# Kernel tuning notes

Hardware: AMD Instinct MI355X
Metric: run time of the kernel (lower is better)

The kernel has to match this reference:

```python
import jax, jax.numpy as jnp
import numpy as np

COST_CLASS, COST_BBOX, COST_GIOU = 1.0, 5.0, 2.0

def box_cxcywh_to_xyxy(b):
    cx, cy, w, h = b[..., 0], b[..., 1], b[..., 2], b[..., 3]
    return jnp.stack([cx - 0.5 * w, cy - 0.5 * h, cx + 0.5 * w, cy + 0.5 * h], axis=-1)

def generalized_box_iou(b1, b2):
    # b1: [bs, Q, 4] xyxy, b2: [bs, T, 4] xyxy -> [bs, Q, T]
    area1 = (b1[..., 2] - b1[..., 0]) * (b1[..., 3] - b1[..., 1])  # [bs,Q]
    area2 = (b2[..., 2] - b2[..., 0]) * (b2[..., 3] - b2[..., 1])  # [bs,T]
    b1e = b1[:, :, None, :]  # [bs,Q,1,4]
    b2e = b2[:, None, :, :]  # [bs,1,T,4]
    lt = jnp.maximum(b1e[..., :2], b2e[..., :2])
    rb = jnp.minimum(b1e[..., 2:], b2e[..., 2:])
    wh = jnp.clip(rb - lt, 0.0)
    inter = wh[..., 0] * wh[..., 1]                       # [bs,Q,T]
    union = area1[:, :, None] + area2[:, None, :] - inter
    iou = inter / union
    # smallest enclosing box
    lt_e = jnp.minimum(b1e[..., :2], b2e[..., :2])
    rb_e = jnp.maximum(b1e[..., 2:], b2e[..., 2:])
    wh_e = jnp.clip(rb_e - lt_e, 0.0)
    area_e = wh_e[..., 0] * wh_e[..., 1]
    return iou - (area_e - union) / area_e

def setup_inputs() -> dict:
    key = jax.random.key(0)
    k1, k2, k3, k4 = jax.random.split(key, 4)
    bs, Q, T, C = 256, 300, 100, 92
    return {
        "pred_logits": jax.random.normal(k1, (bs, Q, C), dtype=jnp.float32),
        "pred_boxes": jax.random.uniform(k2, (bs, Q, 4), dtype=jnp.float32),
        "tgt_labels": jax.random.randint(k3, (bs, T), 0, C),
        "tgt_boxes": jax.random.uniform(k4, (bs, T, 4), dtype=jnp.float32),
    }

def reference(pred_logits, pred_boxes, tgt_labels, tgt_boxes):
    # cost_class: -softmax(logits)[b, q, tgt_labels[b, t]]
    out_prob = jax.nn.softmax(pred_logits, axis=-1)                      # [bs,Q,C]
    cost_class = -jnp.take_along_axis(out_prob, tgt_labels[:, None, :], axis=2)  # [bs,Q,T]
    # cost_bbox: pairwise L1 distance between box coords
    cost_bbox = jnp.sum(jnp.abs(pred_boxes[:, :, None, :] - tgt_boxes[:, None, :, :]), axis=-1)
    # cost_giou: negative generalized IoU in xyxy coords
    cost_giou = -generalized_box_iou(box_cxcywh_to_xyxy(pred_boxes), box_cxcywh_to_xyxy(tgt_boxes))
    C = COST_BBOX * cost_bbox + COST_CLASS * cost_class + COST_GIOU * cost_giou  # [bs,Q,T]
    return C
```

## Files before the change

kernel.cpp:

```cpp
#include <hip/hip_runtime.h>

constexpr int BS = 256;
constexpr int NQ = 300;
constexpr int NT = 100;
constexpr int NC = 92;
constexpr int QT = 60;
constexpr int NTILES = NQ / QT;
constexpr int BLOCK = 256;
constexpr int PSTRIDE = 93;
constexpr int NT4 = NT / 4;

__device__ __forceinline__ float rcpf(float x) { return __builtin_amdgcn_rcpf(x); }

__global__ __launch_bounds__(BLOCK) void matcher_kernel(
    const float* __restrict__ logits,
    const float* __restrict__ pboxes,
    const int*   __restrict__ tlabels,
    const float* __restrict__ tboxes,
    float* __restrict__ out)
{
    __shared__ float  prob[QT * PSTRIDE];
    __shared__ float4 tX0[NT4], tY0[NT4], tX1[NT4], tY1[NT4];
    __shared__ int4   tL[NT4];
    __shared__ float4 p_xy[QT];

    const int b    = blockIdx.x / NTILES;
    const int q0   = (blockIdx.x % NTILES) * QT;
    const int tid  = threadIdx.x;
    const int lane = tid & 63;
    const int wave = tid >> 6;

    if (tid < NT) {
        const float4 tb = *(const float4*)(tboxes + ((size_t)b * NT + tid) * 4);
        ((float*)tX0)[tid] = tb.x - 0.5f * tb.z;
        ((float*)tY0)[tid] = tb.y - 0.5f * tb.w;
        ((float*)tX1)[tid] = tb.x + 0.5f * tb.z;
        ((float*)tY1)[tid] = tb.y + 0.5f * tb.w;
        ((int*)tL)[tid]    = tlabels[(size_t)b * NT + tid];
    } else if (tid >= 128 && tid < 128 + QT) {
        const int q = tid - 128;
        const float4 pb = *(const float4*)(pboxes + ((size_t)b * NQ + q0 + q) * 4);
        p_xy[q] = make_float4(pb.x - 0.5f * pb.z, pb.y - 0.5f * pb.w,
                              pb.x + 0.5f * pb.z, pb.y + 0.5f * pb.w);
    }

    const float* lbase = logits + ((size_t)b * NQ + q0) * NC;
    const int rsub = lane >> 4;
    const int c0   = lane & 15;
    for (int g = wave; g < QT / 4; g += 4) {
        const int q = g * 4 + rsub;
        const float* lr = lbase + (size_t)q * NC;
        float e[6];
        float s = 0.0f;
        #pragma unroll
        for (int k = 0; k < 6; ++k) {
            const int c = c0 + 16 * k;
            e[k] = (c < NC) ? __expf(lr[c]) : 0.0f;
            s += e[k];
        }
        s += __shfl_xor(s, 1);
        s += __shfl_xor(s, 2);
        s += __shfl_xor(s, 4);
        s += __shfl_xor(s, 8);
        const float rs = rcpf(s);
        #pragma unroll
        for (int k = 0; k < 6; ++k) {
            const int c = c0 + 16 * k;
            if (c < NC) prob[q * PSTRIDE + c] = e[k] * rs;
        }
    }
    __syncthreads();

    float4* otile4 = (float4*)(out + ((size_t)b * NQ + q0) * NT);
    for (int idx4 = tid; idx4 < (QT / 2) * NT4; idx4 += BLOCK) {
        const int q  = idx4 / NT4;
        const int t4 = idx4 - q * NT4;

        const float4 x0 = tX0[t4], y0 = tY0[t4], x1 = tX1[t4], y1 = tY1[t4];
        const int4   lb = tL[t4];
        const float tax[4] = {x0.x, x0.y, x0.z, x0.w};
        const float tay[4] = {y0.x, y0.y, y0.z, y0.w};
        const float tbx[4] = {x1.x, x1.y, x1.z, x1.w};
        const float tby[4] = {y1.x, y1.y, y1.z, y1.w};
        const int   lab[4] = {lb.x, lb.y, lb.z, lb.w};
        float tar[4];
        #pragma unroll
        for (int j = 0; j < 4; ++j) tar[j] = (tbx[j] - tax[j]) * (tby[j] - tay[j]);

        #pragma unroll
        for (int h = 0; h < 2; ++h) {
            const int qq = q + h * (QT / 2);
            const float4 p  = p_xy[qq];
            const float par = (p.z - p.x) * (p.w - p.y);
            float plab[4];
            #pragma unroll
            for (int j = 0; j < 4; ++j) plab[j] = prob[qq * PSTRIDE + lab[j]];

            float4 res;
            float* rp = (float*)&res;
            #pragma unroll
            for (int j = 0; j < 4; ++j) {
                const float ax0 = p.x - tax[j], ax1 = p.z - tbx[j];
                const float ay0 = p.y - tay[j], ay1 = p.w - tby[j];
                const float bb = fmaf(0.5f, fabsf(ax0 + ax1), fabsf(ax1 - ax0))
                               + fmaf(0.5f, fabsf(ay0 + ay1), fabsf(ay1 - ay0));
                const float iw = fmaxf(fminf(p.z, tbx[j]) - fmaxf(p.x, tax[j]), 0.0f);
                const float ih = fmaxf(fminf(p.w, tby[j]) - fmaxf(p.y, tay[j]), 0.0f);
                const float inter = iw * ih;
                const float uni = par + tar[j] - inter;
                const float iou = inter * rcpf(uni);
                const float ew = fmaxf(p.z, tbx[j]) - fminf(p.x, tax[j]);
                const float eh = fmaxf(p.w, tby[j]) - fminf(p.y, tay[j]);
                const float ea = ew * eh;
                const float k = (ea - uni) * rcpf(ea);
                rp[j] = fmaf(2.0f, k - iou, fmaf(5.0f, bb, -plab[j]));
            }
            otile4[qq * NT4 + t4] = res;
        }
    }
}

extern "C" void kernel_launch(void* const* d_in, const int* in_sizes, int n_in,
                              void* d_out, int out_size, void* d_ws, size_t ws_size,
                              hipStream_t stream) {
    const float* logits  = (const float*)d_in[0];
    const float* pboxes  = (const float*)d_in[1];
    const int*   tlabels = (const int*)d_in[2];
    const float* tboxes  = (const float*)d_in[3];
    float* out = (float*)d_out;
    matcher_kernel<<<dim3(BS * NTILES), dim3(BLOCK), 0, stream>>>(
        logits, pboxes, tlabels, tboxes, out);
}
```

Measured before the change: 21.18 us.

## Fuse softmax and cost computation per wave using private prob buffers

Replaces the block-wide softmax phase, barrier and separate cost phase with a per-wave flow. Each group of 16 lanes computes the softmax for one query row into a wave-private shared buffer and immediately computes that row's costs, so the second block barrier goes away. Target areas are also precomputed in shared memory, and the GIoU term is rewritten algebraically to drop one subtraction. The risk is lane idling: 15 rows per wave across 4 groups of 4 leaves one slot empty, and 25 float4 outputs across 32 lanes wastes some lanes. The per-row softmax recompute pattern also changes the memory access timing.

```diff
diff --git a/kernel.cpp b/kernel.cpp
--- a/kernel.cpp
+++ b/kernel.cpp
@@ -7,8 +7,9 @@
 constexpr int QT = 60;
 constexpr int NTILES = NQ / QT;
 constexpr int BLOCK = 256;
-constexpr int PSTRIDE = 93;
 constexpr int NT4 = NT / 4;
+constexpr int RPW = QT / 4;
+constexpr int PSTR = 96;
 
 __device__ __forceinline__ float rcpf(float x) { return __builtin_amdgcn_rcpf(x); }
 
@@ -19,10 +20,10 @@
     const float* __restrict__ tboxes,
     float* __restrict__ out)
 {
-    __shared__ float  prob[QT * PSTRIDE];
-    __shared__ float4 tX0[NT4], tY0[NT4], tX1[NT4], tY1[NT4];
+    __shared__ float4 tX0[NT4], tY0[NT4], tX1[NT4], tY1[NT4], tAr[NT4];
     __shared__ int4   tL[NT4];
     __shared__ float4 p_xy[QT];
+    __shared__ float  prob[4][4 * PSTR];
 
     const int b    = blockIdx.x / NTILES;
     const int q0   = (blockIdx.x % NTILES) * QT;
@@ -36,6 +37,7 @@
         ((float*)tY0)[tid] = tb.y - 0.5f * tb.w;
         ((float*)tX1)[tid] = tb.x + 0.5f * tb.z;
         ((float*)tY1)[tid] = tb.y + 0.5f * tb.w;
+        ((float*)tAr)[tid] = tb.z * tb.w;
         ((int*)tL)[tid]    = tlabels[(size_t)b * NT + tid];
     } else if (tid >= 128 && tid < 128 + QT) {
         const int q = tid - 128;
@@ -43,79 +45,81 @@
         p_xy[q] = make_float4(pb.x - 0.5f * pb.z, pb.y - 0.5f * pb.w,
                               pb.x + 0.5f * pb.z, pb.y + 0.5f * pb.w);
     }
+    __syncthreads();
 
-    const float* lbase = logits + ((size_t)b * NQ + q0) * NC;
-    const int rsub = lane >> 4;
-    const int c0   = lane & 15;
-    for (int g = wave; g < QT / 4; g += 4) {
-        const int q = g * 4 + rsub;
-        const float* lr = lbase + (size_t)q * NC;
-        float e[6];
-        float s = 0.0f;
+    const int r   = lane >> 4;
+    const int c16 = lane & 15;
+    const float* lrow0 = logits + ((size_t)b * NQ + q0 + wave * RPW) * NC;
+    float* prow = &prob[wave][r * PSTR];
+
+    for (int g = 0; g < 4; ++g) {
+        const int rg = g * 4 + r;
+        const bool rvalid = (rg < RPW);
+        const int rgc = rvalid ? rg : RPW - 1;
+
+        const float* lr = lrow0 + (size_t)rgc * NC;
+        float e[6]; float s = 0.0f;
         #pragma unroll
         for (int k = 0; k < 6; ++k) {
-            const int c = c0 + 16 * k;
+            const int c = c16 + 16 * k;
             e[k] = (c < NC) ? __expf(lr[c]) : 0.0f;
             s += e[k];
         }
-        s += __shfl_xor(s, 1);
-        s += __shfl_xor(s, 2);
-        s += __shfl_xor(s, 4);
-        s += __shfl_xor(s, 8);
+        s += __shfl_xor(s, 1); s += __shfl_xor(s, 2);
+        s += __shfl_xor(s, 4); s += __shfl_xor(s, 8);
         const float rs = rcpf(s);
         #pragma unroll
         for (int k = 0; k < 6; ++k) {
-            const int c = c0 + 16 * k;
-            if (c < NC) prob[q * PSTRIDE + c] = e[k] * rs;
+            const int c = c16 + 16 * k;
+            if (c < NC) prow[c] = e[k] * rs;
         }
-    }
-    __syncthreads();
+        asm volatile("" ::: "memory");
 
-    float4* otile4 = (float4*)(out + ((size_t)b * NQ + q0) * NT);
-    for (int idx4 = tid; idx4 < (QT / 2) * NT4; idx4 += BLOCK) {
-        const int q  = idx4 / NT4;
-        const int t4 = idx4 - q * NT4;
-
-        const float4 x0 = tX0[t4], y0 = tY0[t4], x1 = tX1[t4], y1 = tY1[t4];
-        const int4   lb = tL[t4];
-        const float tax[4] = {x0.x, x0.y, x0.z, x0.w};
-        const float tay[4] = {y0.x, y0.y, y0.z, y0.w};
-        const float tbx[4] = {x1.x, x1.y, x1.z, x1.w};
-        const float tby[4] = {y1.x, y1.y, y1.z, y1.w};
-        const int   lab[4] = {lb.x, lb.y, lb.z, lb.w};
-        float tar[4];
-        #pragma unroll
-        for (int j = 0; j < 4; ++j) tar[j] = (tbx[j] - tax[j]) * (tby[j] - tay[j]);
+        const int qrow = wave * RPW + rgc;
+        const float4 P = p_xy[qrow];
+        const float par = (P.z - P.x) * (P.w - P.y);
+        float* orow = out + ((size_t)b * NQ + q0 + qrow) * NT;
 
         #pragma unroll
-        for (int h = 0; h < 2; ++h) {
-            const int qq = q + h * (QT / 2);
-            const float4 p  = p_xy[qq];
-            const float par = (p.z - p.x) * (p.w - p.y);
-            float plab[4];
+        for (int pass = 0; pass < 2; ++pass) {
+            const int tq  = c16 + 16 * pass;
+            const bool act = rvalid && (tq < NT4);
+            const int tqc = (tq < NT4) ? tq : 0;
+
+            const float4 x0 = tX0[tqc], y0 = tY0[tqc], x1 = tX1[tqc], y1 = tY1[tqc];
+            const float4 ar = tAr[tqc];
+            const int4   lb = tL[tqc];
+            const float tax[4] = {x0.x, x0.y, x0.z, x0.w};
+            const float tay[4] = {y0.x, y0.y, y0.z, y0.w};
+            const float tbx[4] = {x1.x, x1.y, x1.z, x1.w};
+            const float tby[4] = {y1.x, y1.y, y1.z, y1.w};
+            const float tar[4] = {ar.x, ar.y, ar.z, ar.w};
+            const int  labs[4] = {lb.x, lb.y, lb.z, lb.w};
+
+            float pl[4];
             #pragma unroll
-            for (int j = 0; j < 4; ++j) plab[j] = prob[qq * PSTRIDE + lab[j]];
+            for (int u = 0; u < 4; ++u) pl[u] = prow[labs[u]];
 
-            float4 res;
-            float* rp = (float*)&res;
+            float4 res; float* rp = (float*)&res;
             #pragma unroll
-            for (int j = 0; j < 4; ++j) {
-                const float ax0 = p.x - tax[j], ax1 = p.z - tbx[j];
-                const float ay0 = p.y - tay[j], ay1 = p.w - tby[j];
+            for (int u = 0; u < 4; ++u) {
+                const float ax0 = P.x - tax[u], ax1 = P.z - tbx[u];
+                const float ay0 = P.y - tay[u], ay1 = P.w - tby[u];
                 const float bb = fmaf(0.5f, fabsf(ax0 + ax1), fabsf(ax1 - ax0))
                                + fmaf(0.5f, fabsf(ay0 + ay1), fabsf(ay1 - ay0));
-                const float iw = fmaxf(fminf(p.z, tbx[j]) - fmaxf(p.x, tax[j]), 0.0f);
-                const float ih = fmaxf(fminf(p.w, tby[j]) - fmaxf(p.y, tay[j]), 0.0f);
+                const float dx = fminf(P.z, tbx[u]) - fmaxf(P.x, tax[u]);
+                const float dy = fminf(P.w, tby[u]) - fmaxf(P.y, tay[u]);
+                const float iw = fmaxf(dx, 0.0f), ih = fmaxf(dy, 0.0f);
                 const float inter = iw * ih;
-                const float uni = par + tar[j] - inter;
+                const float uni = (par + tar[u]) - inter;
+                const float ew = fmaxf(P.z, tbx[u]) - fminf(P.x, tax[u]);
+                const float eh = fmaxf(P.w, tby[u]) - fminf(P.y, tay[u]);
+                const float ea = ew * eh;
                 const float iou = inter * rcpf(uni);
-                const float ew = fmaxf(p.z, tbx[j]) - fminf(p.x, tax[j]);
-                const float eh = fmaxf(p.w, tby[j]) - fminf(p.y, tay[j]);
-                const float ea = ew * eh;
-                const float k = (ea - uni) * rcpf(ea);
-                rp[j] = fmaf(2.0f, k - iou, fmaf(5.0f, bb, -plab[j]));
+                const float ur  = uni * rcpf(ea);
+                rp[u] = fmaf(-2.0f, ur, fmaf(-2.0f, iou, fmaf(5.0f, bb, 2.0f - pl[u])));
             }
-            otile4[qq * NT4 + t4] = res;
+            if (act) *(float4*)(orow + 4 * tq) = res;
         }
     }
 }
```

Result: slower. 22.56 us (+6.5%).
